# Kernel optimization log

Measured on AMD Instinct MI355X. Metric: run time of the kernel, lower is better.

The kernel has to match this reference:

```python
import jax, jax.numpy as jnp
import numpy as np

NEG = -1000000000.0
TEMP = 0.5
K = 15
EPS = 1e-5


def _bn(x, g, b):
    # BatchNorm1d in training mode: batch mean, biased variance
    mu = jnp.mean(x, axis=0)
    var = jnp.mean((x - mu) ** 2, axis=0)
    return (x - mu) * jax.lax.rsqrt(var + EPS) * g + b


def _lrelu(x):
    return jnp.where(x > 0, x, 0.2 * x)


def setup_inputs() -> dict:
    key = jax.random.key(0)
    ks = jax.random.split(key, 8)
    B, L = 131072, 50
    inp = {
        "z": jax.random.normal(ks[0], (B, L), jnp.float32),
        "u": jax.random.uniform(ks[1], (K, B, 25), jnp.float32),
        "W1": jax.random.normal(ks[2], (L, 128), jnp.float32) * 0.1,
        "b1": jnp.zeros((128,), jnp.float32),
        "g1": jnp.ones((128,), jnp.float32),
        "be1": jnp.zeros((128,), jnp.float32),
        "W2": jax.random.normal(ks[3], (128, 256), jnp.float32) * 0.1,
        "b2": jnp.zeros((256,), jnp.float32),
        "g2": jnp.ones((256,), jnp.float32),
        "be2": jnp.zeros((256,), jnp.float32),
        "W3": jax.random.normal(ks[4], (256, 128), jnp.float32) * 0.1,
        "b3": jnp.zeros((128,), jnp.float32),
        "g3": jnp.ones((128,), jnp.float32),
        "be3": jnp.zeros((128,), jnp.float32),
        "W4": jax.random.normal(ks[5], (128, 25), jnp.float32) * 0.1,
        "b4": jnp.zeros((25,), jnp.float32),
    }
    return inp


def reference(z, u, W1, b1, g1, be1, W2, b2, g2, be2, W3, b3, g3, be3, W4, b4):
    h = _lrelu(_bn(z @ W1 + b1, g1, be1))
    h = _lrelu(_bn(h @ W2 + b2, g2, be2))
    h = _lrelu(_bn(h @ W3 + b3, g3, be3))
    logits = h @ W4 + b4  # [B, 25]

    def step(mask, u_i):
        masked = jnp.where(mask, logits, NEG)
        noise = -jnp.log(-jnp.log(u_i))
        gumbel = (masked + noise) / TEMP
        probs = jax.nn.softmax(gumbel, axis=-1)
        idx = jnp.argmax(probs, axis=-1)  # [B]
        onehot = jax.nn.one_hot(idx, 25, dtype=bool)
        return mask & ~onehot, idx

    mask0 = jnp.ones(logits.shape, dtype=bool)
    _, idxs = jax.lax.scan(step, mask0, u)  # idxs: [K, B]
    selected = idxs.T.astype(jnp.float32) + 1.0  # [B, K], selected_idx + 1
    return (selected - 1.0) / 24.0
```

## Files before the change

### kernel.cpp

```cpp
#include <hip/hip_runtime.h>
#include <math.h>

#define BATCH 131072

template<int MT, int NT, int NSTORE, int TM, int TN, int BLK, int KS, int K,
         bool AFFINE, bool STATS>
__global__ __launch_bounds__(BLK)
void gemm_bn2(const float* __restrict__ Ain, const float* __restrict__ W,
              const float* __restrict__ bias,
              const float* __restrict__ gamma, const float* __restrict__ beta,
              const double* __restrict__ prevSum, const double* __restrict__ prevSq,
              float* __restrict__ Xout_g,
              double* __restrict__ outSum, double* __restrict__ outSq)
{
    constexpr int KC   = (K + KS - 1) / KS;
    constexpr bool TAIL = (K % KS) != 0;
    constexpr int CPR  = KS / 4;
    constexpr int NCG  = NT / TN;
    constexpr int RG   = MT / TM;
    constexpr int NH   = TN / 4;
    constexpr int AL4  = MT * KS / 4 / BLK;
    constexpr bool BVEC = (NT == NSTORE);
    constexpr int BL4  = BVEC ? (KS * NT / 4 / BLK) : 1;
    constexpr int BLS  = BVEC ? 1 : (KS * NT / BLK);
    constexpr int HF   = (TM >= 8) ? 8 : TM;
    static_assert(NCG * RG == BLK, "thread mapping");
    static_assert(TM % HF == 0, "half split");
    static_assert(!STATS || 2 * RG * NT <= KS * NT, "stats scratch fits Bs");

    __shared__ float As[MT][KS];
    __shared__ float Bs[KS][NT];
    __shared__ float scs[AFFINE ? K : 1];
    __shared__ float shs[AFFINE ? K : 1];

    const int tid = threadIdx.x;
    const int r0  = blockIdx.x * MT;
    const int tx  = tid % NCG;
    const int ty  = tid / NCG;
    const int key = ty & 3;

    if constexpr (AFFINE) {
        for (int i = tid; i < K; i += BLK) {
            const double inv = 1.0 / (double)BATCH;
            double mu  = prevSum[i] * inv;
            double var = prevSq[i] * inv - mu * mu;
            double s   = (double)gamma[i] / sqrt(var + 1e-5);
            scs[i] = (float)s;
            shs[i] = (float)((double)beta[i] - mu * s);
        }
    }

    float acc[TM][TN] = {};

    for (int kc = 0; kc < KC; ++kc) {
        const int kb = kc * KS;
        __syncthreads();
        #pragma unroll
        for (int l = 0; l < AL4; ++l) {
            int idx = tid + l * BLK;
            int row = idx / CPR;
            int c4  = idx % CPR;
            int gk  = kb + c4 * 4;
            const float* gp = Ain + (size_t)(r0 + row) * K + gk;
            float4 v;
            if constexpr (!TAIL) {
                v = *reinterpret_cast<const float4*>(gp);
            } else {
                if (gk + 4 <= K) v = *reinterpret_cast<const float4*>(gp);
                else {
                    float tt[4];
                    #pragma unroll
                    for (int c = 0; c < 4; ++c) tt[c] = (gk + c < K) ? gp[c] : 0.f;
                    v = make_float4(tt[0], tt[1], tt[2], tt[3]);
                }
            }
            if constexpr (AFFINE) {
                float* vp = &v.x;
                #pragma unroll
                for (int c = 0; c < 4; ++c) {
                    float x = vp[c] * scs[gk + c] + shs[gk + c];
                    vp[c] = x > 0.f ? x : 0.2f * x;
                }
            }
            *reinterpret_cast<float4*>(&As[row][(c4 ^ ((row / TM) & 3)) * 4]) = v;
        }
        if constexpr (BVEC) {
            #pragma unroll
            for (int l = 0; l < BL4; ++l) {
                int idx = tid + l * BLK;
                int kk  = idx / (NT / 4);
                int n4  = idx % (NT / 4);
                int gk  = kb + kk;
                float4 v;
                if constexpr (!TAIL)
                    v = *reinterpret_cast<const float4*>(W + (size_t)gk * NSTORE + n4 * 4);
                else
                    v = (gk < K)
                      ? *reinterpret_cast<const float4*>(W + (size_t)gk * NSTORE + n4 * 4)
                      : make_float4(0.f, 0.f, 0.f, 0.f);
                *reinterpret_cast<float4*>(&Bs[kk][n4 * 4]) = v;
            }
        } else {
            #pragma unroll
            for (int l = 0; l < BLS; ++l) {
                int idx = tid + l * BLK;
                int kk  = idx / NT;
                int n   = idx % NT;
                int gk  = kb + kk;
                Bs[kk][n] = (gk < K && n < NSTORE) ? W[(size_t)gk * NSTORE + n] : 0.f;
            }
        }
        __syncthreads();
        #pragma unroll
        for (int k4 = 0; k4 < CPR; ++k4) {
            const int pf = (k4 ^ key) * 4;
            float4 bq[4][NH];
            #pragma unroll
            for (int kk = 0; kk < 4; ++kk)
                #pragma unroll
                for (int h = 0; h < NH; ++h)
                    bq[kk][h] = *reinterpret_cast<const float4*>(
                        &Bs[k4 * 4 + kk][h * (NCG * 4) + tx * 4]);
            #pragma unroll
            for (int hf = 0; hf < TM / HF; ++hf) {
                float4 a4[HF];
                #pragma unroll
                for (int i = 0; i < HF; ++i)
                    a4[i] = *reinterpret_cast<const float4*>(
                        &As[ty * TM + hf * HF + i][pf]);
                #pragma unroll
                for (int kk = 0; kk < 4; ++kk)
                    #pragma unroll
                    for (int i = 0; i < HF; ++i) {
                        const float av = (&a4[i].x)[kk];
                        const float* bp = &bq[kk][0].x;
                        #pragma unroll
                        for (int j = 0; j < TN; ++j)
                            acc[hf * HF + i][j] = fmaf(av, bp[j], acc[hf * HF + i][j]);
                    }
            }
        }
    }

    float bc[TN];
    #pragma unroll
    for (int j = 0; j < TN; ++j) {
        int gc = (j >> 2) * (NCG * 4) + tx * 4 + (j & 3);
        bc[j] = (gc < NSTORE) ? bias[gc] : 0.f;
    }
    float psum[TN] = {}, psq[TN] = {};
    #pragma unroll
    for (int i = 0; i < TM; ++i) {
        int row = r0 + ty * TM + i;
        float x[TN];
        #pragma unroll
        for (int j = 0; j < TN; ++j) {
            x[j] = acc[i][j] + bc[j];
            if (STATS) { psum[j] += x[j]; psq[j] += x[j] * x[j]; }
        }
        if constexpr (BVEC) {
            #pragma unroll
            for (int h = 0; h < NH; ++h) {
                float4 v = make_float4(x[h*4], x[h*4+1], x[h*4+2], x[h*4+3]);
                *reinterpret_cast<float4*>(
                    &Xout_g[(size_t)row * NSTORE + h * (NCG * 4) + tx * 4]) = v;
            }
        } else {
            #pragma unroll
            for (int j = 0; j < TN; ++j) {
                int gc = (j >> 2) * (NCG * 4) + tx * 4 + (j & 3);
                if (gc < NSTORE) Xout_g[(size_t)row * NSTORE + gc] = x[j];
            }
        }
    }
    if constexpr (STATS) {
        __syncthreads();
        float* S1 = &Bs[0][0];
        float* S2 = S1 + RG * NT;
        #pragma unroll
        for (int j = 0; j < TN; ++j) {
            int gc = (j >> 2) * (NCG * 4) + tx * 4 + (j & 3);
            S1[ty * NT + gc] = psum[j];
            S2[ty * NT + gc] = psq[j];
        }
        __syncthreads();
        if (tid < NT) {
            double s = 0.0, q = 0.0;
            #pragma unroll 4
            for (int t = 0; t < RG; ++t) {
                s += (double)S1[t * NT + tid];
                q += (double)S2[t * NT + tid];
            }
            atomicAdd(&outSum[tid], s);
            atomicAdd(&outSq[tid], q);
        }
    }
}

__global__ __launch_bounds__(256)
void gumbel_topk(const float* __restrict__ logits, const float* __restrict__ u,
                 float* __restrict__ out)
{
    __shared__ __align__(16) float lg[256 * 25];
    __shared__ __align__(16) float us[2][256 * 25];
    const int tid = threadIdx.x;
    const int r0  = blockIdx.x * 256;

    {
        const float4* src = reinterpret_cast<const float4*>(logits + (size_t)r0 * 25);
        float4* dst = reinterpret_cast<float4*>(lg);
        #pragma unroll
        for (int l = 0; l < 7; ++l) {
            int i = tid + l * 256;
            if (i < 1600) dst[i] = src[i];
        }
        const float4* u0 = reinterpret_cast<const float4*>(u + (size_t)r0 * 25);
        float4* d0 = reinterpret_cast<float4*>(us[0]);
        #pragma unroll
        for (int l = 0; l < 7; ++l) {
            int i = tid + l * 256;
            if (i < 1600) d0[i] = u0[i];
        }
    }
    __syncthreads();

    float myl[25];
    #pragma unroll
    for (int j = 0; j < 25; ++j) myl[j] = lg[tid * 25 + j];

    unsigned mask = 0x1FFFFFFu;
    for (int it = 0; it < 15; ++it) {
        const int cur = it & 1;
        float4 t[7];
        const bool have = (it + 1) < 15;
        if (have) {
            const float4* un = reinterpret_cast<const float4*>(
                u + ((size_t)(it + 1) * BATCH + r0) * 25);
            #pragma unroll
            for (int l = 0; l < 7; ++l) {
                int i = tid + l * 256;
                if (i < 1600) t[l] = un[i];
            }
        }

        float best = -INFINITY;
        int bj = 0;
        #pragma unroll
        for (int j = 0; j < 25; ++j) {
            float uu = us[cur][tid * 25 + j];
            float nz = -logf(-logf(uu));
            float v  = myl[j] + nz;
            v = ((mask >> j) & 1u) ? v : -INFINITY;
            if (v > best) { best = v; bj = j; }
        }
        mask &= ~(1u << bj);
        out[(size_t)(r0 + tid) * 15 + it] = (float)bj / 24.0f;

        if (have) {
            float4* dn = reinterpret_cast<float4*>(us[cur ^ 1]);
            #pragma unroll
            for (int l = 0; l < 7; ++l) {
                int i = tid + l * 256;
                if (i < 1600) dn[i] = t[l];
            }
        }
        __syncthreads();
    }
}

extern "C" void kernel_launch(void* const* d_in, const int* in_sizes, int n_in,
                              void* d_out, int out_size, void* d_ws, size_t ws_size,
                              hipStream_t stream)
{
    (void)in_sizes; (void)n_in; (void)out_size; (void)ws_size;
    const float* z   = (const float*)d_in[0];
    const float* u   = (const float*)d_in[1];
    const float* W1  = (const float*)d_in[2];
    const float* b1  = (const float*)d_in[3];
    const float* g1  = (const float*)d_in[4];
    const float* be1 = (const float*)d_in[5];
    const float* W2  = (const float*)d_in[6];
    const float* b2  = (const float*)d_in[7];
    const float* g2  = (const float*)d_in[8];
    const float* be2 = (const float*)d_in[9];
    const float* W3  = (const float*)d_in[10];
    const float* b3  = (const float*)d_in[11];
    const float* g3  = (const float*)d_in[12];
    const float* be3 = (const float*)d_in[13];
    const float* W4  = (const float*)d_in[14];
    const float* b4  = (const float*)d_in[15];
    float* out = (float*)d_out;

    char* ws = (char*)d_ws;
    float* X2     = (float*)ws;
    float* XA     = (float*)(ws + (size_t)134217728);
    char*  statb  = ws + (size_t)134217728 + (size_t)67108864;
    double* sum1 = (double*)statb;      double* sq1 = sum1 + 128;
    double* sum2 = sq1 + 128;           double* sq2 = sum2 + 256;
    double* sum3 = sq2 + 256;           double* sq3 = sum3 + 128;
    float* logits = X2;

    (void)hipMemsetAsync(statb, 0, 1024 * sizeof(double), stream);

    gemm_bn2<256,128,128, 16,8, 256, 32, 50, false, true>
        <<<BATCH/256, 256, 0, stream>>>(z, W1, b1, nullptr, nullptr,
                                        nullptr, nullptr, XA, sum1, sq1);

    gemm_bn2<128,256,256, 16,8, 256, 32, 128, true, true>
        <<<BATCH/128, 256, 0, stream>>>(XA, W2, b2, g1, be1,
                                        sum1, sq1, X2, sum2, sq2);

    gemm_bn2<256,128,128, 16,8, 256, 32, 256, true, true>
        <<<BATCH/256, 256, 0, stream>>>(X2, W3, b3, g2, be2,
                                        sum2, sq2, XA, sum3, sq3);

    gemm_bn2<256,32,25, 4,8, 256, 32, 128, true, false>
        <<<BATCH/256, 256, 0, stream>>>(XA, W4, b4, g3, be3,
                                        sum3, sq3, logits, nullptr, nullptr);

    gumbel_topk<<<BATCH/256, 256, 0, stream>>>(logits, u, out);
}
```

Measured before the change: 738.6 us.

## Double-buffer GEMM shared-memory tiles with register prefetch and smaller K-slice

```diff
diff --git a/kernel.cpp b/kernel.cpp
--- a/kernel.cpp
+++ b/kernel.cpp
@@ -6,7 +6,7 @@
 template<int MT, int NT, int NSTORE, int TM, int TN, int BLK, int KS, int K,
          bool AFFINE, bool STATS>
 __global__ __launch_bounds__(BLK)
-void gemm_bn2(const float* __restrict__ Ain, const float* __restrict__ W,
+void gemm_bn3(const float* __restrict__ Ain, const float* __restrict__ W,
               const float* __restrict__ bias,
               const float* __restrict__ gamma, const float* __restrict__ beta,
               const double* __restrict__ prevSum, const double* __restrict__ prevSq,
@@ -20,16 +20,17 @@
     constexpr int RG   = MT / TM;
     constexpr int NH   = TN / 4;
     constexpr int AL4  = MT * KS / 4 / BLK;
-    constexpr bool BVEC = (NT == NSTORE);
+    constexpr bool BVEC = (NT == NSTORE) && (KS * NT / 4 >= BLK);
     constexpr int BL4  = BVEC ? (KS * NT / 4 / BLK) : 1;
     constexpr int BLS  = BVEC ? 1 : (KS * NT / BLK);
     constexpr int HF   = (TM >= 8) ? 8 : TM;
     static_assert(NCG * RG == BLK, "thread mapping");
-    static_assert(TM % HF == 0, "half split");
-    static_assert(!STATS || 2 * RG * NT <= KS * NT, "stats scratch fits Bs");
-
-    __shared__ float As[MT][KS];
-    __shared__ float Bs[KS][NT];
+    static_assert(MT * KS / 4 % BLK == 0, "A staging divisibility");
+    static_assert(CPR == 4, "swizzle assumes 4 groups");
+    static_assert(!STATS || RG <= KS, "stats scratch fits Bs");
+
+    __shared__ float As[2][MT][KS];
+    __shared__ float Bs[2][KS][NT];
     __shared__ float scs[AFFINE ? K : 1];
     __shared__ float shs[AFFINE ? K : 1];
 
@@ -51,30 +52,64 @@
     }
 
     float acc[TM][TN] = {};
-
-    for (int kc = 0; kc < KC; ++kc) {
-        const int kb = kc * KS;
-        __syncthreads();
+    float4 aReg[AL4];
+    float4 bReg[BVEC ? BL4 : 1];
+    float  bRegS[BVEC ? 1 : BLS];
+
+    auto issue = [&](int kc) {
         #pragma unroll
         for (int l = 0; l < AL4; ++l) {
             int idx = tid + l * BLK;
             int row = idx / CPR;
             int c4  = idx % CPR;
-            int gk  = kb + c4 * 4;
+            int gk  = kc * KS + c4 * 4;
             const float* gp = Ain + (size_t)(r0 + row) * K + gk;
-            float4 v;
             if constexpr (!TAIL) {
-                v = *reinterpret_cast<const float4*>(gp);
+                aReg[l] = *reinterpret_cast<const float4*>(gp);
             } else {
-                if (gk + 4 <= K) v = *reinterpret_cast<const float4*>(gp);
+                if (gk + 4 <= K) aReg[l] = *reinterpret_cast<const float4*>(gp);
                 else {
                     float tt[4];
                     #pragma unroll
                     for (int c = 0; c < 4; ++c) tt[c] = (gk + c < K) ? gp[c] : 0.f;
-                    v = make_float4(tt[0], tt[1], tt[2], tt[3]);
+                    aReg[l] = make_float4(tt[0], tt[1], tt[2], tt[3]);
                 }
             }
+        }
+        if constexpr (BVEC) {
+            #pragma unroll
+            for (int l = 0; l < BL4; ++l) {
+                int idx = tid + l * BLK;
+                int kk  = idx / (NT / 4);
+                int n4  = idx % (NT / 4);
+                int gk  = kc * KS + kk;
+                if constexpr (!TAIL)
+                    bReg[l] = *reinterpret_cast<const float4*>(W + (size_t)gk * NSTORE + n4 * 4);
+                else
+                    bReg[l] = (gk < K)
+                        ? *reinterpret_cast<const float4*>(W + (size_t)gk * NSTORE + n4 * 4)
+                        : make_float4(0.f, 0.f, 0.f, 0.f);
+            }
+        } else {
+            #pragma unroll
+            for (int l = 0; l < BLS; ++l) {
+                int idx = tid + l * BLK;
+                int kk  = idx / NT;
+                int n   = idx % NT;
+                int gk  = kc * KS + kk;
+                bRegS[l] = (gk < K && n < NSTORE) ? W[(size_t)gk * NSTORE + n] : 0.f;
+            }
+        }
+    };
+    auto commit = [&](int kc, int d) {
+        #pragma unroll
+        for (int l = 0; l < AL4; ++l) {
+            int idx = tid + l * BLK;
+            int row = idx / CPR;
+            int c4  = idx % CPR;
+            float4 v = aReg[l];
             if constexpr (AFFINE) {
+                int gk = kc * KS + c4 * 4;
                 float* vp = &v.x;
                 #pragma unroll
                 for (int c = 0; c < 4; ++c) {
@@ -82,35 +117,23 @@
                     vp[c] = x > 0.f ? x : 0.2f * x;
                 }
             }
-            *reinterpret_cast<float4*>(&As[row][(c4 ^ ((row / TM) & 3)) * 4]) = v;
+            *reinterpret_cast<float4*>(&As[d][row][(c4 ^ ((row / TM) & 3)) * 4]) = v;
         }
         if constexpr (BVEC) {
             #pragma unroll
             for (int l = 0; l < BL4; ++l) {
                 int idx = tid + l * BLK;
-                int kk  = idx / (NT / 4);
-                int n4  = idx % (NT / 4);
-                int gk  = kb + kk;
-                float4 v;
-                if constexpr (!TAIL)
-                    v = *reinterpret_cast<const float4*>(W + (size_t)gk * NSTORE + n4 * 4);
-                else
-                    v = (gk < K)
-                      ? *reinterpret_cast<const float4*>(W + (size_t)gk * NSTORE + n4 * 4)
-                      : make_float4(0.f, 0.f, 0.f, 0.f);
-                *reinterpret_cast<float4*>(&Bs[kk][n4 * 4]) = v;
+                *reinterpret_cast<float4*>(&Bs[d][idx / (NT / 4)][(idx % (NT / 4)) * 4]) = bReg[l];
             }
         } else {
             #pragma unroll
             for (int l = 0; l < BLS; ++l) {
                 int idx = tid + l * BLK;
-                int kk  = idx / NT;
-                int n   = idx % NT;
-                int gk  = kb + kk;
-                Bs[kk][n] = (gk < K && n < NSTORE) ? W[(size_t)gk * NSTORE + n] : 0.f;
-            }
-        }
-        __syncthreads();
+                Bs[d][idx / NT][idx % NT] = bRegS[l];
+            }
+        }
+    };
+    auto compute = [&](int d) {
         #pragma unroll
         for (int k4 = 0; k4 < CPR; ++k4) {
             const int pf = (k4 ^ key) * 4;
@@ -120,14 +143,14 @@
                 #pragma unroll
                 for (int h = 0; h < NH; ++h)
                     bq[kk][h] = *reinterpret_cast<const float4*>(
-                        &Bs[k4 * 4 + kk][h * (NCG * 4) + tx * 4]);
+                        &Bs[d][k4 * 4 + kk][h * (NCG * 4) + tx * 4]);
             #pragma unroll
             for (int hf = 0; hf < TM / HF; ++hf) {
                 float4 a4[HF];
                 #pragma unroll
                 for (int i = 0; i < HF; ++i)
                     a4[i] = *reinterpret_cast<const float4*>(
-                        &As[ty * TM + hf * HF + i][pf]);
+                        &As[d][ty * TM + hf * HF + i][pf]);
                 #pragma unroll
                 for (int kk = 0; kk < 4; ++kk)
                     #pragma unroll
@@ -140,6 +163,17 @@
                     }
             }
         }
+    };
+
+    issue(0);
+    __syncthreads();
+    commit(0, 0);
+    #pragma unroll 1
+    for (int kc = 0; kc < KC; ++kc) {
+        if (kc + 1 < KC) issue(kc + 1);
+        __syncthreads();
+        compute(kc & 1);
+        if (kc + 1 < KC) commit(kc + 1, (kc + 1) & 1);
     }
 
     float bc[TN];
@@ -158,7 +192,7 @@
             x[j] = acc[i][j] + bc[j];
             if (STATS) { psum[j] += x[j]; psq[j] += x[j] * x[j]; }
         }
-        if constexpr (BVEC) {
+        if constexpr (NT == NSTORE) {
             #pragma unroll
             for (int h = 0; h < NH; ++h) {
                 float4 v = make_float4(x[h*4], x[h*4+1], x[h*4+2], x[h*4+3]);
@@ -175,7 +209,7 @@
     }
     if constexpr (STATS) {
         __syncthreads();
-        float* S1 = &Bs[0][0];
+        float* S1 = &Bs[0][0][0];
         float* S2 = S1 + RG * NT;
         #pragma unroll
         for (int j = 0; j < TN; ++j) {
@@ -302,19 +336,19 @@
 
     (void)hipMemsetAsync(statb, 0, 1024 * sizeof(double), stream);
 
-    gemm_bn2<256,128,128, 16,8, 256, 32, 50, false, true>
+    gemm_bn3<256,128,128, 16,8, 256, 16, 50, false, true>
         <<<BATCH/256, 256, 0, stream>>>(z, W1, b1, nullptr, nullptr,
                                         nullptr, nullptr, XA, sum1, sq1);
 
-    gemm_bn2<128,256,256, 16,8, 256, 32, 128, true, true>
+    gemm_bn3<128,256,256, 16,8, 256, 16, 128, true, true>
         <<<BATCH/128, 256, 0, stream>>>(XA, W2, b2, g1, be1,
                                         sum1, sq1, X2, sum2, sq2);
 
-    gemm_bn2<256,128,128, 16,8, 256, 32, 256, true, true>
+    gemm_bn3<256,128,128, 16,8, 256, 16, 256, true, true>
         <<<BATCH/256, 256, 0, stream>>>(X2, W3, b3, g2, be2,
                                         sum2, sq2, XA, sum3, sq3);
 
-    gemm_bn2<256,32,25, 4,8, 256, 32, 128, true, false>
+    gemm_bn3<256,32,25, 4,8, 256, 16, 128, true, false>
         <<<BATCH/256, 256, 0, stream>>>(XA, W4, b4, g3, be3,
                                         sum3, sq3, logits, nullptr, nullptr);
 
```

Result: slower. 1.274 ms (+72.5%).

## Double-buffer GEMM tiles with async global-to-LDS loads and split out BN pass

Applied to the files above, without the earlier changes.

```diff
diff --git a/kernel.cpp b/kernel.cpp
--- a/kernel.cpp
+++ b/kernel.cpp
@@ -1,37 +1,39 @@
 #include <hip/hip_runtime.h>
 #include <math.h>
+#include <stdint.h>
 
 #define BATCH 131072
 
+typedef __attribute__((address_space(3))) uint32_t lds_u32_t;
+typedef const __attribute__((address_space(1))) uint32_t gbl_u32_t;
+__device__ __forceinline__ void gload16(const float* g, float* l) {
+    __builtin_amdgcn_global_load_lds((gbl_u32_t*)g, (lds_u32_t*)l, 16, 0, 0);
+}
+
 template<int MT, int NT, int NSTORE, int TM, int TN, int BLK, int KS, int K,
-         bool AFFINE, bool STATS>
+         bool STATS, bool BFULL>
 __global__ __launch_bounds__(BLK)
-void gemm_bn2(const float* __restrict__ Ain, const float* __restrict__ W,
-              const float* __restrict__ bias,
-              const float* __restrict__ gamma, const float* __restrict__ beta,
-              const double* __restrict__ prevSum, const double* __restrict__ prevSq,
-              float* __restrict__ Xout_g,
-              double* __restrict__ outSum, double* __restrict__ outSq)
-{
-    constexpr int KC   = (K + KS - 1) / KS;
-    constexpr bool TAIL = (K % KS) != 0;
-    constexpr int CPR  = KS / 4;
-    constexpr int NCG  = NT / TN;
-    constexpr int RG   = MT / TM;
-    constexpr int NH   = TN / 4;
-    constexpr int AL4  = MT * KS / 4 / BLK;
-    constexpr bool BVEC = (NT == NSTORE);
-    constexpr int BL4  = BVEC ? (KS * NT / 4 / BLK) : 1;
-    constexpr int BLS  = BVEC ? 1 : (KS * NT / BLK);
-    constexpr int HF   = (TM >= 8) ? 8 : TM;
+void gemm_ld(const float* __restrict__ Ain, const float* __restrict__ W,
+             const float* __restrict__ bias, float* __restrict__ Xout,
+             double* __restrict__ outSum, double* __restrict__ outSq)
+{
+    constexpr int KC  = K / KS;
+    constexpr int CPR = KS / 4;
+    constexpr int NCG = NT / TN;
+    constexpr int RG  = MT / TM;
+    constexpr int NH  = TN / 4;
+    constexpr int AL4 = MT * KS / 4 / BLK;
+    constexpr int BL4 = BFULL ? 1 : (KS * NT / 4 / BLK);
+    constexpr int HF  = (TM >= 8) ? 8 : TM;
+    static_assert(K % KS == 0, "no K tail in gemm_ld");
     static_assert(NCG * RG == BLK, "thread mapping");
-    static_assert(TM % HF == 0, "half split");
-    static_assert(!STATS || 2 * RG * NT <= KS * NT, "stats scratch fits Bs");
-
-    __shared__ float As[MT][KS];
-    __shared__ float Bs[KS][NT];
-    __shared__ float scs[AFFINE ? K : 1];
-    __shared__ float shs[AFFINE ? K : 1];
+    static_assert((MT * KS / 4) % BLK == 0, "A staging divisibility");
+    static_assert(CPR == 4, "swizzle assumes 4 groups/row");
+    static_assert(!STATS || 2 * RG * NT <= 2 * KS * NT, "stats scratch fits Bs");
+
+    __shared__ float As[2][MT][KS];
+    __shared__ float Bs[BFULL ? 1 : 2][KS][NT];
+    __shared__ float Bf[BFULL ? K : 1][BFULL ? NT : 1];
 
     const int tid = threadIdx.x;
     const int r0  = blockIdx.x * MT;
@@ -39,78 +41,30 @@
     const int ty  = tid / NCG;
     const int key = ty & 3;
 
-    if constexpr (AFFINE) {
-        for (int i = tid; i < K; i += BLK) {
-            const double inv = 1.0 / (double)BATCH;
-            double mu  = prevSum[i] * inv;
-            double var = prevSq[i] * inv - mu * mu;
-            double s   = (double)gamma[i] / sqrt(var + 1e-5);
-            scs[i] = (float)s;
-            shs[i] = (float)((double)beta[i] - mu * s);
-        }
-    }
-
     float acc[TM][TN] = {};
 
-    for (int kc = 0; kc < KC; ++kc) {
-        const int kb = kc * KS;
-        __syncthreads();
+    auto stageA = [&](int kc, int d) {
         #pragma unroll
         for (int l = 0; l < AL4; ++l) {
             int idx = tid + l * BLK;
             int row = idx / CPR;
-            int c4  = idx % CPR;
-            int gk  = kb + c4 * 4;
-            const float* gp = Ain + (size_t)(r0 + row) * K + gk;
-            float4 v;
-            if constexpr (!TAIL) {
-                v = *reinterpret_cast<const float4*>(gp);
-            } else {
-                if (gk + 4 <= K) v = *reinterpret_cast<const float4*>(gp);
-                else {
-                    float tt[4];
-                    #pragma unroll
-                    for (int c = 0; c < 4; ++c) tt[c] = (gk + c < K) ? gp[c] : 0.f;
-                    v = make_float4(tt[0], tt[1], tt[2], tt[3]);
-                }
-            }
-            if constexpr (AFFINE) {
-                float* vp = &v.x;
-                #pragma unroll
-                for (int c = 0; c < 4; ++c) {
-                    float x = vp[c] * scs[gk + c] + shs[gk + c];
-                    vp[c] = x > 0.f ? x : 0.2f * x;
-                }
-            }
-            *reinterpret_cast<float4*>(&As[row][(c4 ^ ((row / TM) & 3)) * 4]) = v;
-        }
-        if constexpr (BVEC) {
-            #pragma unroll
-            for (int l = 0; l < BL4; ++l) {
-                int idx = tid + l * BLK;
-                int kk  = idx / (NT / 4);
-                int n4  = idx % (NT / 4);
-                int gk  = kb + kk;
-                float4 v;
-                if constexpr (!TAIL)
-                    v = *reinterpret_cast<const float4*>(W + (size_t)gk * NSTORE + n4 * 4);
-                else
-                    v = (gk < K)
-                      ? *reinterpret_cast<const float4*>(W + (size_t)gk * NSTORE + n4 * 4)
-                      : make_float4(0.f, 0.f, 0.f, 0.f);
-                *reinterpret_cast<float4*>(&Bs[kk][n4 * 4]) = v;
-            }
-        } else {
-            #pragma unroll
-            for (int l = 0; l < BLS; ++l) {
-                int idx = tid + l * BLK;
-                int kk  = idx / NT;
-                int n   = idx % NT;
-                int gk  = kb + kk;
-                Bs[kk][n] = (gk < K && n < NSTORE) ? W[(size_t)gk * NSTORE + n] : 0.f;
-            }
-        }
-        __syncthreads();
+            int p   = idx % CPR;
+            int c4  = p ^ ((row / TM) & 3);
+            gload16(Ain + (size_t)(r0 + row) * K + kc * KS + c4 * 4,
+                    &As[d][0][0] + idx * 4);
+        }
+    };
+    auto stageB = [&](int kc, int d) {
+        #pragma unroll
+        for (int l = 0; l < BL4; ++l) {
+            int idx = tid + l * BLK;
+            int kk  = idx / (NT / 4);
+            int n4  = idx % (NT / 4);
+            gload16(W + (size_t)(kc * KS + kk) * NSTORE + n4 * 4,
+                    &Bs[d][0][0] + idx * 4);
+        }
+    };
+    auto compute = [&](int kb, int d) {
         #pragma unroll
         for (int k4 = 0; k4 < CPR; ++k4) {
             const int pf = (k4 ^ key) * 4;
@@ -120,14 +74,15 @@
                 #pragma unroll
                 for (int h = 0; h < NH; ++h)
                     bq[kk][h] = *reinterpret_cast<const float4*>(
-                        &Bs[k4 * 4 + kk][h * (NCG * 4) + tx * 4]);
+                        BFULL ? &Bf[kb + k4 * 4 + kk][h * (NCG * 4) + tx * 4]
+                              : &Bs[d][k4 * 4 + kk][h * (NCG * 4) + tx * 4]);
             #pragma unroll
             for (int hf = 0; hf < TM / HF; ++hf) {
                 float4 a4[HF];
                 #pragma unroll
                 for (int i = 0; i < HF; ++i)
                     a4[i] = *reinterpret_cast<const float4*>(
-                        &As[ty * TM + hf * HF + i][pf]);
+                        &As[d][ty * TM + hf * HF + i][pf]);
                 #pragma unroll
                 for (int kk = 0; kk < 4; ++kk)
                     #pragma unroll
@@ -140,6 +95,32 @@
                     }
             }
         }
+    };
+
+    stageA(0, 0);
+    if constexpr (BFULL) {
+        constexpr int BLSF = K * NT / BLK;
+        #pragma unroll
+        for (int l = 0; l < BLSF; ++l) {
+            int idx = tid + l * BLK;
+            int kk  = idx / NT;
+            int n   = idx % NT;
+            Bf[kk][n] = (n < NSTORE) ? W[(size_t)kk * NSTORE + n] : 0.f;
+        }
+    } else {
+        stageB(0, 0);
+    }
+    __syncthreads();
+
+    #pragma unroll 1
+    for (int kc = 0; kc < KC; ++kc) {
+        const int d = kc & 1;
+        if (kc + 1 < KC) {
+            stageA(kc + 1, d ^ 1);
+            if constexpr (!BFULL) stageB(kc + 1, d ^ 1);
+        }
+        compute(kc * KS, d);
+        __syncthreads();
     }
 
     float bc[TN];
@@ -158,24 +139,24 @@
             x[j] = acc[i][j] + bc[j];
             if (STATS) { psum[j] += x[j]; psq[j] += x[j] * x[j]; }
         }
-        if constexpr (BVEC) {
+        if constexpr (NT == NSTORE) {
             #pragma unroll
             for (int h = 0; h < NH; ++h) {
                 float4 v = make_float4(x[h*4], x[h*4+1], x[h*4+2], x[h*4+3]);
                 *reinterpret_cast<float4*>(
-                    &Xout_g[(size_t)row * NSTORE + h * (NCG * 4) + tx * 4]) = v;
+                    &Xout[(size_t)row * NSTORE + h * (NCG * 4) + tx * 4]) = v;
             }
         } else {
             #pragma unroll
             for (int j = 0; j < TN; ++j) {
                 int gc = (j >> 2) * (NCG * 4) + tx * 4 + (j & 3);
-                if (gc < NSTORE) Xout_g[(size_t)row * NSTORE + gc] = x[j];
+                if (gc < NSTORE) Xout[(size_t)row * NSTORE + gc] = x[j];
             }
         }
     }
     if constexpr (STATS) {
         __syncthreads();
-        float* S1 = &Bs[0][0];
+        float* S1 = &Bs[0][0][0];
         float* S2 = S1 + RG * NT;
         #pragma unroll
         for (int j = 0; j < TN; ++j) {
@@ -194,6 +175,68 @@
             atomicAdd(&outSum[tid], s);
             atomicAdd(&outSq[tid], q);
         }
+    }
+}
+
+__global__ void finalize_bn(const double* __restrict__ sum, const double* __restrict__ sq,
+                            const float* __restrict__ g, const float* __restrict__ be,
+                            float* __restrict__ sc, float* __restrict__ sh, int N)
+{
+    int i = threadIdx.x;
+    if (i < N) {
+        const double inv = 1.0 / (double)BATCH;
+        double mu  = sum[i] * inv;
+        double var = sq[i] * inv - mu * mu;
+        double s   = (double)g[i] / sqrt(var + 1e-5);
+        sc[i] = (float)s;
+        sh[i] = (float)((double)be[i] - mu * s);
+    }
+}
+
+__global__ __launch_bounds__(256)
+void bn_lrelu(float* __restrict__ X, const float* __restrict__ sc,
+              const float* __restrict__ sh, int C4, size_t n4)
+{
+    size_t i = (size_t)blockIdx.x * 256 + threadIdx.x;
+    const size_t stride = (size_t)gridDim.x * 256;
+    for (; i < n4; i += stride) {
+        int c4 = (int)(i % (size_t)C4);
+        float4 v = reinterpret_cast<float4*>(X)[i];
+        float4 s = reinterpret_cast<const float4*>(sc)[c4];
+        float4 h = reinterpret_cast<const float4*>(sh)[c4];
+        float* vp = &v.x; const float* sp = &s.x; const float* hp = &h.x;
+        #pragma unroll
+        for (int c = 0; c < 4; ++c) {
+            float x = vp[c] * sp[c] + hp[c];
+            vp[c] = x > 0.f ? x : 0.2f * x;
+        }
+        reinterpret_cast<float4*>(X)[i] = v;
+    }
+}
+
+__global__ __launch_bounds__(256)
+void pad_z(const float* __restrict__ z, float* __restrict__ Z64)
+{
+    size_t i = (size_t)blockIdx.x * 256 + threadIdx.x;
+    const size_t stride = (size_t)gridDim.x * 256;
+    const size_t n4 = (size_t)BATCH * 16;
+    for (; i < n4; i += stride) {
+        size_t row = i / 16;
+        int c0 = (int)(i % 16) * 4;
+        float t[4];
+        #pragma unroll
+        for (int c = 0; c < 4; ++c)
+            t[c] = (c0 + c < 50) ? z[row * 50 + c0 + c] : 0.f;
+        reinterpret_cast<float4*>(Z64)[i] = make_float4(t[0], t[1], t[2], t[3]);
+    }
+}
+
+__global__ __launch_bounds__(256)
+void pad_w1(const float* __restrict__ W1, float* __restrict__ W1p)
+{
+    for (int idx = threadIdx.x; idx < 64 * 128; idx += 256) {
+        int r = idx / 128;
+        W1p[idx] = (r < 50) ? W1[idx] : 0.f;
     }
 }
 
@@ -292,31 +335,41 @@
     float* out = (float*)d_out;
 
     char* ws = (char*)d_ws;
-    float* X2     = (float*)ws;
-    float* XA     = (float*)(ws + (size_t)134217728);
-    char*  statb  = ws + (size_t)134217728 + (size_t)67108864;
-    double* sum1 = (double*)statb;      double* sq1 = sum1 + 128;
+    float* X2   = (float*)ws;
+    float* XA   = (float*)(ws + (size_t)134217728);
+    char*  aux  = ws + (size_t)134217728 + (size_t)67108864;
+    double* sum1 = (double*)aux;        double* sq1 = sum1 + 128;
     double* sum2 = sq1 + 128;           double* sq2 = sum2 + 256;
     double* sum3 = sq2 + 256;           double* sq3 = sum3 + 128;
+    float* sc1 = (float*)(aux + 8192);  float* sh1 = sc1 + 128;
+    float* sc2 = sh1 + 128;             float* sh2 = sc2 + 256;
+    float* sc3 = sh2 + 256;             float* sh3 = sc3 + 128;
+    float* W1p = (float*)(aux + 16384);
+    float* Z64 = X2;
     float* logits = X2;
 
-    (void)hipMemsetAsync(statb, 0, 1024 * sizeof(double), stream);
-
-    gemm_bn2<256,128,128, 16,8, 256, 32, 50, false, true>
-        <<<BATCH/256, 256, 0, stream>>>(z, W1, b1, nullptr, nullptr,
-                                        nullptr, nullptr, XA, sum1, sq1);
-
-    gemm_bn2<128,256,256, 16,8, 256, 32, 128, true, true>
-        <<<BATCH/128, 256, 0, stream>>>(XA, W2, b2, g1, be1,
-                                        sum1, sq1, X2, sum2, sq2);
-
-    gemm_bn2<256,128,128, 16,8, 256, 32, 256, true, true>
-        <<<BATCH/256, 256, 0, stream>>>(X2, W3, b3, g2, be2,
-                                        sum2, sq2, XA, sum3, sq3);
-
-    gemm_bn2<256,32,25, 4,8, 256, 32, 128, true, false>
-        <<<BATCH/256, 256, 0, stream>>>(XA, W4, b4, g3, be3,
-                                        sum3, sq3, logits, nullptr, nullptr);
+    (void)hipMemsetAsync(aux, 0, 1024 * sizeof(double), stream);
+
+    pad_z<<<2048, 256, 0, stream>>>(z, Z64);
+    pad_w1<<<1, 256, 0, stream>>>(W1, W1p);
+
+    gemm_ld<256,128,128, 16,8, 256, 16, 64, true, false>
+        <<<BATCH/256, 256, 0, stream>>>(Z64, W1p, b1, XA, sum1, sq1);
+    finalize_bn<<<1, 256, 0, stream>>>(sum1, sq1, g1, be1, sc1, sh1, 128);
+    bn_lrelu<<<2048, 256, 0, stream>>>(XA, sc1, sh1, 32, (size_t)BATCH * 32);
+
+    gemm_ld<128,256,256, 16,8, 256, 16, 128, true, false>
+        <<<BATCH/128, 256, 0, stream>>>(XA, W2, b2, X2, sum2, sq2);
+    finalize_bn<<<1, 256, 0, stream>>>(sum2, sq2, g2, be2, sc2, sh2, 256);
+    bn_lrelu<<<2048, 256, 0, stream>>>(X2, sc2, sh2, 64, (size_t)BATCH * 64);
+
+    gemm_ld<256,128,128, 16,8, 256, 16, 256, true, false>
+        <<<BATCH/256, 256, 0, stream>>>(X2, W3, b3, XA, sum3, sq3);
+    finalize_bn<<<1, 256, 0, stream>>>(sum3, sq3, g3, be3, sc3, sh3, 128);
+    bn_lrelu<<<2048, 256, 0, stream>>>(XA, sc3, sh3, 32, (size_t)BATCH * 32);
+
+    gemm_ld<256,32,25, 4,8, 256, 16, 128, false, true>
+        <<<BATCH/256, 256, 0, stream>>>(XA, W4, b4, logits, nullptr, nullptr);
 
     gumbel_topk<<<BATCH/256, 256, 0, stream>>>(logits, u, out);
 }
```

New measurement: 856.6 us. 16.0% more time.
